# Performance work log

Measured on AMD Instinct MI355X. Metric: run time of the kernel, lower is better.

Reference implementation:

```python
import jax, jax.numpy as jnp
import numpy as np

NUM_NODES = 12288
NUM_GRAPHS = 1024
LEADS_PER_GRAPH = 12
SIG_LEN = 2048
NUM_EDGES = 196608


def _conv1d(x, w, b, stride, pad):
    # x: [N, C_in, L], w: [C_out, C_in, K]
    y = jax.lax.conv_general_dilated(
        x, w, window_strides=(stride,), padding=[(pad, pad)],
        dimension_numbers=("NCH", "OIH", "NCH"))
    return y + b[None, :, None]


def _gcn(x, src, dst, W, b, n_nodes):
    # PyG GCNConv: add self-loops, symmetric deg^-1/2 normalization.
    h = x @ W  # [N, out]
    loop = jnp.arange(n_nodes, dtype=src.dtype)
    s = jnp.concatenate([src, loop])
    d = jnp.concatenate([dst, loop])
    deg = jax.ops.segment_sum(jnp.ones(d.shape, h.dtype), d, num_segments=n_nodes)
    dis = jax.lax.rsqrt(deg)  # deg >= 1 due to self-loops
    norm = dis[s] * dis[d]  # [E+N]
    return jax.ops.segment_sum(h[s] * norm[:, None], d, num_segments=n_nodes) + b


def setup_inputs() -> dict:
    key = jax.random.key(0)
    ks = jax.random.split(key, 16)
    f = jnp.float32
    inp = {
        "x_raw": jax.random.normal(ks[0], (NUM_NODES, SIG_LEN), f),
        "conv1_w": jax.random.normal(ks[1], (16, 1, 7), f) * 0.2,
        "conv1_b": jax.random.normal(ks[2], (16,), f) * 0.05,
        "conv2_w": jax.random.normal(ks[3], (32, 16, 5), f) * 0.1,
        "conv2_b": jax.random.normal(ks[4], (32,), f) * 0.05,
        "lin_w": jax.random.normal(ks[5], (32, 64), f) * 0.15,
        "lin_b": jax.random.normal(ks[6], (64,), f) * 0.05,
        "gnn1_w": jax.random.normal(ks[7], (64, 128), f) * 0.1,
        "gnn1_b": jax.random.normal(ks[8], (128,), f) * 0.05,
        "gnn2_w": jax.random.normal(ks[9], (128, 128), f) * 0.08,
        "gnn2_b": jax.random.normal(ks[10], (128,), f) * 0.05,
        "fc_w": jax.random.normal(ks[11], (128, 5), f) * 0.08,
        "fc_b": jax.random.normal(ks[12], (5,), f) * 0.05,
        "edge_index": jax.random.randint(ks[13], (2, NUM_EDGES), 0, NUM_NODES, jnp.int32),
        "batch": (jnp.arange(NUM_NODES, dtype=jnp.int32) // LEADS_PER_GRAPH),
        "num_graphs": NUM_GRAPHS,
    }
    return inp


def reference(x_raw, conv1_w, conv1_b, conv2_w, conv2_b, lin_w, lin_b,
              gnn1_w, gnn1_b, gnn2_w, gnn2_b, fc_w, fc_b,
              edge_index, batch, num_graphs):
    n_nodes = x_raw.shape[0]
    # LeadCNN encoder
    h = x_raw[:, None, :]                              # [N,1,L]
    h = jax.nn.relu(_conv1d(h, conv1_w, conv1_b, 2, 3))  # [N,16,L/2]
    h = jax.nn.relu(_conv1d(h, conv2_w, conv2_b, 2, 2))  # [N,32,L/4]
    h = jnp.mean(h, axis=-1)                           # AdaptiveAvgPool1d(1)
    h = h @ lin_w + lin_b                              # [N,cnn_out]
    # Two GCN layers with ReLU
    src, dst = edge_index[0], edge_index[1]
    h = jax.nn.relu(_gcn(h, src, dst, gnn1_w, gnn1_b, n_nodes))
    h = jax.nn.relu(_gcn(h, src, dst, gnn2_w, gnn2_b, n_nodes))
    # global_mean_pool over batch
    sums = jax.ops.segment_sum(h, batch, num_segments=num_graphs)
    cnts = jax.ops.segment_sum(jnp.ones((n_nodes,), h.dtype), batch, num_segments=num_graphs)
    pooled = sums / jnp.maximum(cnts, 1.0)[:, None]
    return pooled @ fc_w + fc_b
```

## Files before the change

kernel.cpp:

```cpp
#include <hip/hip_runtime.h>
#include <cstddef>

#define N_NODES 12288
#define SIG     2048
#define C1N     16
#define L1N     1024
#define C2N     32
#define F0      64
#define F1      128
#define NEDGE   196608
#define NGRAPH  1024

#define NB_ENC   (N_NODES / 2)
#define CNT_BLKS (NEDGE / 256 + N_NODES / 256)

typedef float    f32x4 __attribute__((ext_vector_type(4)));
typedef _Float16 f16x8 __attribute__((ext_vector_type(8)));
typedef _Float16 f16x4 __attribute__((ext_vector_type(4)));
typedef __fp16   fp16x2_raw __attribute__((ext_vector_type(2)));

#if defined(__has_builtin)
#if __has_builtin(__builtin_amdgcn_mfma_f32_16x16x16f16)
#define HAVE_MFMA16 1
#endif
#endif

__device__ __forceinline__ unsigned pkrtz(float a, float b) {
    union { fp16x2_raw h; unsigned u; } c;
    c.h = __builtin_amdgcn_cvt_pkrtz(a, b);
    return c.u;
}

__global__ __launch_bounds__(256) void k_encoder(
    const float* __restrict__ x_raw,
    const float* __restrict__ conv1_w, const float* __restrict__ conv1_b,
    const float* __restrict__ conv2_w, const float* __restrict__ conv2_b,
    const float* __restrict__ lin_w,   const float* __restrict__ lin_b,
    float* __restrict__ h0,
    const int* __restrict__ dst, const int* __restrict__ batch,
    int* __restrict__ deg, float* __restrict__ cnt)
{
    __shared__ __align__(16) unsigned xw[2][1056];
    __shared__ __align__(16) unsigned c1t[4 * 800];
    __shared__ float wmsum[4][C2N];
    __shared__ float mean_s[2][C2N];

    const int tid = threadIdx.x;

    if (blockIdx.x >= NB_ENC) {
        const int b = blockIdx.x - NB_ENC;
        if (b < NEDGE / 256) {
            atomicAdd(&deg[dst[b * 256 + tid]], 1);
        } else {
            atomicAdd(&cnt[batch[(b - NEDGE / 256) * 256 + tid]], 1.f);
        }
        return;
    }

    const int lane = tid & 63;
    const int wq   = tid >> 6;
    const int colL = lane & 15;
    const int hi8  = lane >> 4;
    const int ndl  = wq >> 1;
    const int hf   = wq & 1;
    const int node = blockIdx.x * 2 + ndl;
    const float* xrow = x_raw + (size_t)node * SIG;
    unsigned* xn = &xw[ndl][0];

    const int nqu = hf ? 132 : 136;
    #pragma unroll
    for (int it = 0; it < 3; ++it) {
        int i = lane + 64 * it;
        if (i < nqu) {
            int xb = 1024 * hf + 8 * i - 8;
            float v[8];
            if (xb >= 0 && xb + 8 <= SIG) {
                float4 xa = *(const float4*)(xrow + xb);
                float4 xc = *(const float4*)(xrow + xb + 4);
                v[0] = xa.x; v[1] = xa.y; v[2] = xa.z; v[3] = xa.w;
                v[4] = xc.x; v[5] = xc.y; v[6] = xc.z; v[7] = xc.w;
            } else {
                #pragma unroll
                for (int t = 0; t < 8; ++t) {
                    int xi = xb + t;
                    v[t] = ((unsigned)xi < (unsigned)SIG) ? xrow[xi] : 0.f;
                }
            }
            uint4 w4;
            w4.x = pkrtz(v[0], v[1]); w4.y = pkrtz(v[2], v[3]);
            w4.z = pkrtz(v[4], v[5]); w4.w = pkrtz(v[6], v[7]);
            *(uint4*)&xn[512 * hf + 4 * i] = w4;
        }
    }
    if (hf == 1 && lane < 16) xn[1040 + lane] = 0u;

#if HAVE_MFMA16
    f16x4 w1A;
    #pragma unroll
    for (int j = 0; j < 4; ++j) w1A[j] = (_Float16)0.f;
    if (hi8 == 0) {
        #pragma unroll
        for (int j = 1; j < 4; ++j) w1A[j] = (_Float16)conv1_w[colL * 7 + (j - 1)];
    } else if (hi8 == 1) {
        #pragma unroll
        for (int j = 0; j < 4; ++j) w1A[j] = (_Float16)conv1_w[colL * 7 + 3 + j];
    }
#else
    f16x8 w1A;
    #pragma unroll
    for (int j = 0; j < 8; ++j) w1A[j] = (_Float16)0.f;
    if (hi8 == 0) {
        #pragma unroll
        for (int j = 1; j < 8; ++j) w1A[j] = (_Float16)conv1_w[colL * 7 + (j - 1)];
    }
#endif
    float bias1[4];
    #pragma unroll
    for (int r = 0; r < 4; ++r) bias1[r] = conv1_b[hi8 * 4 + r];

    f16x8 wA[2][3];
    #pragma unroll
    for (int mt = 0; mt < 2; ++mt) {
        const int oc = mt * 16 + colL;
        #pragma unroll
        for (int kt = 0; kt < 3; ++kt) {
            #pragma unroll
            for (int j = 0; j < 8; ++j) {
                const int ic  = 4 * hi8 + (j & 3);
                const int tap = 2 * kt + (j >> 2);
                wA[mt][kt][j] = (_Float16)((tap < 5) ? conv2_w[oc * 80 + ic * 5 + tap] : 0.f);
            }
        }
    }
    float bias2[2][4];
    #pragma unroll
    for (int mt = 0; mt < 2; ++mt)
        #pragma unroll
        for (int r = 0; r < 4; ++r)
            bias2[mt][r] = conv2_b[mt * 16 + hi8 * 4 + r];

    float msumr[2][4];
    #pragma unroll
    for (int mt = 0; mt < 2; ++mt)
        #pragma unroll
        for (int r = 0; r < 4; ++r) msumr[mt][r] = 0.f;

    unsigned* cw = &c1t[wq * 800];
    const int rb = 20 * colL + 4 * hi8;

    #pragma unroll 1
    for (int sp = 0; sp < 8; ++sp) {
        const int xwb = 512 * hf + 64 * sp;

        #pragma unroll
        for (int T = 0; T < 5; ++T) {
            f32x4 a;
            a[0] = bias1[0]; a[1] = bias1[1]; a[2] = bias1[2]; a[3] = bias1[3];
#if HAVE_MFMA16
            const int wbase = xwb + 16 * T + colL + 2 * hi8;
            union { unsigned u[2]; f16x4 v; } Bx;
            Bx.u[0] = xn[wbase];
            Bx.u[1] = xn[wbase + 1];
            a = __builtin_amdgcn_mfma_f32_16x16x16f16(w1A, Bx.v, a, 0, 0, 0);
#else
            const int wbase = xwb + 16 * T + colL + 4 * hi8;
            union { unsigned u[4]; f16x8 v; } Bx;
            #pragma unroll
            for (int u = 0; u < 4; ++u) Bx.u[u] = xn[wbase + u];
            a = __builtin_amdgcn_mfma_f32_16x16x32_f16(w1A, Bx.v, a, 0, 0, 0);
#endif
            uint2 wr;
            wr.x = pkrtz(fmaxf(a[0], 0.f), fmaxf(a[1], 0.f));
            wr.y = pkrtz(fmaxf(a[2], 0.f), fmaxf(a[3], 0.f));
            const int slot = 16 * T + colL;
            *(uint2*)&cw[(slot >> 1) * 20 + 4 * hi8 + (slot & 1) * 2] = wr;
        }
        if (hf == 0 && sp == 0) {
            if (lane < 16) cw[lane] = 0u;
        }
        if (hf == 1 && sp == 7) {
            for (int k2 = lane; k2 < 140; k2 += 64) cw[660 + k2] = 0u;
        }

        #pragma unroll
        for (int nt = 0; nt < 2; ++nt) {
            f32x4 acc[2];
            #pragma unroll
            for (int mt = 0; mt < 2; ++mt) {
                acc[mt][0] = bias2[mt][0]; acc[mt][1] = bias2[mt][1];
                acc[mt][2] = bias2[mt][2]; acc[mt][3] = bias2[mt][3];
            }
            #pragma unroll
            for (int kt = 0; kt < 3; ++kt) {
                union { uint4 u4; f16x8 v; } B;
                B.u4 = *(const uint4*)&cw[rb + 320 * nt + 20 * kt];
                #pragma unroll
                for (int mt = 0; mt < 2; ++mt)
                    acc[mt] = __builtin_amdgcn_mfma_f32_16x16x32_f16(wA[mt][kt], B.v, acc[mt], 0, 0, 0);
            }
            #pragma unroll
            for (int mt = 0; mt < 2; ++mt)
                #pragma unroll
                for (int r = 0; r < 4; ++r)
                    msumr[mt][r] += fmaxf(acc[mt][r], 0.f);
        }
    }

    #pragma unroll
    for (int mt = 0; mt < 2; ++mt)
        #pragma unroll
        for (int r = 0; r < 4; ++r) {
            float s = msumr[mt][r];
            s += __shfl_xor(s, 1);
            s += __shfl_xor(s, 2);
            s += __shfl_xor(s, 4);
            s += __shfl_xor(s, 8);
            msumr[mt][r] = s;
        }
    if (colL == 0) {
        #pragma unroll
        for (int mt = 0; mt < 2; ++mt)
            #pragma unroll
            for (int r = 0; r < 4; ++r)
                wmsum[wq][mt * 16 + hi8 * 4 + r] = msumr[mt][r];
    }
    __syncthreads();

    if (tid < 64) {
        const int nd2 = tid >> 5, oc = tid & 31;
        mean_s[nd2][oc] = (wmsum[2 * nd2][oc] + wmsum[2 * nd2 + 1][oc]) * (1.f / 512.f);
    }
    __syncthreads();

    if (tid < 128) {
        const int nd2 = tid >> 6, o = tid & 63;
        const int nodew = blockIdx.x * 2 + nd2;
        float a = lin_b[o];
        #pragma unroll
        for (int ic = 0; ic < C2N; ++ic)
            a = fmaf(mean_s[nd2][ic], lin_w[ic * F0 + o], a);
        h0[(size_t)nodew * F0 + o] = a;
    }
}

__global__ __launch_bounds__(1024) void k_scan(const int* __restrict__ deg,
                                               int* __restrict__ rowptr,
                                               int* __restrict__ cursor,
                                               float* __restrict__ dis,
                                               float* __restrict__ invd)
{
    __shared__ int wtot[16];
    const int t = threadIdx.x;
    const int lane = t & 63, wvid = t >> 6;
    int d[12]; int s = 0;
    #pragma unroll
    for (int m = 0; m < 12; ++m) { d[m] = deg[12 * t + m]; s += d[m]; }
    const int mysum = s;
    #pragma unroll
    for (int off = 1; off < 64; off <<= 1) {
        int u = __shfl_up(s, off);
        if (lane >= off) s += u;
    }
    if (lane == 63) wtot[wvid] = s;
    __syncthreads();
    if (t < 16) {
        int v = wtot[t];
        #pragma unroll
        for (int off = 1; off < 16; off <<= 1) {
            int u = __shfl_up(v, off);
            if (t >= off) v += u;
        }
        wtot[t] = v;
    }
    __syncthreads();
    int run = (wvid ? wtot[wvid - 1] : 0) + (s - mysum);
    if (t == 0) rowptr[0] = 0;
    #pragma unroll
    for (int m = 0; m < 12; ++m) {
        const int i = 12 * t + m;
        cursor[i] = run;
        run += d[m];
        rowptr[i + 1] = run;
        float df = (float)(d[m] + 1);
        dis[i]  = rsqrtf(df);
        invd[i] = 1.f / df;
    }
}

__global__ __launch_bounds__(256) void k_scatter(const int* __restrict__ src,
                                                 const int* __restrict__ dst,
                                                 int* __restrict__ cursor,
                                                 int* __restrict__ csr)
{
    int e = blockIdx.x * 256 + threadIdx.x;
    if (e < NEDGE) {
        int d = dst[e];
        int idx = atomicAdd(&cursor[d], 1);
        csr[idx] = src[e];
    }
}

template <int K, int POOL>
__global__ __launch_bounds__(256) void k_gcn(
    const float* __restrict__ h, const int* __restrict__ rowptr,
    const int* __restrict__ csr, const float* __restrict__ dis,
    const float* __restrict__ invd, const float* __restrict__ W,
    const float* __restrict__ bvec, float* __restrict__ out,
    const int* __restrict__ batch, float* __restrict__ pooled)
{
    __shared__ float hs[8][K];
    const int tid = threadIdx.x;
    const int n0  = blockIdx.x * 8;

    const int npb = 256 / K;
    const int f   = tid & (K - 1);
    const int sub = tid / K;
    #pragma unroll
    for (int it = 0; it < 8 / npb; ++it) {
        const int nl = it * npb + sub;
        const int n  = n0 + nl;
        const float dn = dis[n];
        float a0 = h[(size_t)n * K + f] * invd[n];
        float a1 = 0.f, a2 = 0.f, a3 = 0.f;
        int e = rowptr[n];
        const int e1 = rowptr[n + 1];
        for (; e + 3 < e1; e += 4) {
            int s0 = csr[e], s1 = csr[e + 1], s2 = csr[e + 2], s3 = csr[e + 3];
            a0 = fmaf(h[(size_t)s0 * K + f], dis[s0] * dn, a0);
            a1 = fmaf(h[(size_t)s1 * K + f], dis[s1] * dn, a1);
            a2 = fmaf(h[(size_t)s2 * K + f], dis[s2] * dn, a2);
            a3 = fmaf(h[(size_t)s3 * K + f], dis[s3] * dn, a3);
        }
        for (; e < e1; ++e) {
            int s0 = csr[e];
            a0 = fmaf(h[(size_t)s0 * K + f], dis[s0] * dn, a0);
        }
        hs[nl][f] = (a0 + a1) + (a2 + a3);
    }
    __syncthreads();

    const int j    = tid & 127;
    const int half = tid >> 7;
    float a[4];
    #pragma unroll
    for (int c = 0; c < 4; ++c) a[c] = bvec[j];

    for (int k4 = 0; k4 < K; k4 += 4) {
        float w0 = W[(k4 + 0) * F1 + j];
        float w1 = W[(k4 + 1) * F1 + j];
        float w2 = W[(k4 + 2) * F1 + j];
        float w3 = W[(k4 + 3) * F1 + j];
        #pragma unroll
        for (int c = 0; c < 4; ++c) {
            float4 hv = *(const float4*)&hs[half * 4 + c][k4];
            a[c] = fmaf(hv.x, w0, a[c]);
            a[c] = fmaf(hv.y, w1, a[c]);
            a[c] = fmaf(hv.z, w2, a[c]);
            a[c] = fmaf(hv.w, w3, a[c]);
        }
    }
    #pragma unroll
    for (int c = 0; c < 4; ++c) {
        float r = fmaxf(a[c], 0.f);
        int n = n0 + half * 4 + c;
        if (POOL) atomicAdd(&pooled[(size_t)batch[n] * F1 + j], r);
        else      out[(size_t)n * F1 + j] = r;
    }
}

__global__ __launch_bounds__(128) void k_final(const float* __restrict__ pooled,
                                               const float* __restrict__ cnt,
                                               const float* __restrict__ fc_w,
                                               const float* __restrict__ fc_b,
                                               float* __restrict__ out)
{
    __shared__ float ps[F1];
    const int g = blockIdx.x, tid = threadIdx.x;
    float inv = 1.f / fmaxf(cnt[g], 1.f);
    ps[tid] = pooled[g * F1 + tid] * inv;
    __syncthreads();
    if (tid < 5) {
        float a = fc_b[tid];
        for (int f = 0; f < F1; ++f) a = fmaf(ps[f], fc_w[f * 5 + tid], a);
        out[g * 5 + tid] = a;
    }
}

extern "C" void kernel_launch(void* const* d_in, const int* in_sizes, int n_in,
                              void* d_out, int out_size, void* d_ws, size_t ws_size,
                              hipStream_t stream)
{
    const float* x_raw = (const float*)d_in[0];
    const float* c1w   = (const float*)d_in[1];
    const float* c1b   = (const float*)d_in[2];
    const float* c2w   = (const float*)d_in[3];
    const float* c2b   = (const float*)d_in[4];
    const float* lw    = (const float*)d_in[5];
    const float* lb    = (const float*)d_in[6];
    const float* g1w   = (const float*)d_in[7];
    const float* g1b   = (const float*)d_in[8];
    const float* g2w   = (const float*)d_in[9];
    const float* g2b   = (const float*)d_in[10];
    const float* fcw   = (const float*)d_in[11];
    const float* fcb   = (const float*)d_in[12];
    const int*   ei    = (const int*)d_in[13];
    const int*   batch = (const int*)d_in[14];
    const int* src = ei;
    const int* dst = ei + NEDGE;

    float* ws = (float*)d_ws;
    float* h0     = ws + 0;
    float* h1     = ws + 786432;
    float* dis    = ws + 2359296;
    float* invd   = ws + 2371584;
    float* pooled = ws + 2383872;
    float* cnt    = ws + 2514944;
    int*   deg    = (int*)(ws + 2515968);
    int*   rowptr = (int*)(ws + 2528256);
    int*   cursor = (int*)(ws + 2540548);
    int*   csr    = (int*)(ws + 2552836);

    float* out = (float*)d_out;

    hipMemsetAsync(deg, 0, N_NODES * sizeof(int), stream);
    hipMemsetAsync(pooled, 0, (size_t)(NGRAPH * F1 + NGRAPH) * sizeof(float), stream);

    k_encoder<<<NB_ENC + CNT_BLKS, 256, 0, stream>>>(
        x_raw, c1w, c1b, c2w, c2b, lw, lb, h0, dst, batch, deg, cnt);
    k_scan<<<1, 1024, 0, stream>>>(deg, rowptr, cursor, dis, invd);
    k_scatter<<<NEDGE / 256, 256, 0, stream>>>(src, dst, cursor, csr);

    k_gcn<F0, 0><<<N_NODES / 8, 256, 0, stream>>>(h0, rowptr, csr, dis, invd, g1w, g1b, h1, batch, pooled);
    k_gcn<F1, 1><<<N_NODES / 8, 256, 0, stream>>>(h1, rowptr, csr, dis, invd, g2w, g2b, nullptr, batch, pooled);

    k_final<<<NGRAPH, 128, 0, stream>>>(pooled, cnt, fcw, fcb, out);
}
```

Before: 154.9 us.

## Store GCN layer-1 output as fp16 and shrink encoder LDS footprint

Layer-1 GCN output is now packed to fp16 pairs, which halves the bytes gathered per edge in the layer-2 aggregation; layer 2 unpacks the pairs and accumulates in fp32. The encoder's conv1 tile buffer shrinks from 800 to 680 words per wave, with the reduction scratch aliased into it behind an added barrier, to cut LDS use and possibly raise occupancy. ReLU after conv1 is applied with a packed fp16 max, and the unused tail tile writes are skipped. The fp16 intermediate adds rounding error to the layer-2 inputs.

Measured after the change: 177.8 us. +14.8%, slower.

```diff
diff --git a/kernel.cpp b/kernel.cpp
--- a/kernel.cpp
+++ b/kernel.cpp
@@ -13,6 +13,7 @@
 
 #define NB_ENC   (N_NODES / 2)
 #define CNT_BLKS (NEDGE / 256 + N_NODES / 256)
+#define C1TW     680
 
 typedef float    f32x4 __attribute__((ext_vector_type(4)));
 typedef _Float16 f16x8 __attribute__((ext_vector_type(8)));
@@ -29,6 +30,18 @@
     union { fp16x2_raw h; unsigned u; } c;
     c.h = __builtin_amdgcn_cvt_pkrtz(a, b);
     return c.u;
+}
+__device__ __forceinline__ unsigned pkmax0(unsigned x) {
+    unsigned r;
+    asm("v_pk_max_f16 %0, %1, 0" : "=v"(r) : "v"(x));
+    return r;
+}
+__device__ __forceinline__ unsigned short f16_bits(float f) {
+    union { _Float16 h; unsigned short u; } c; c.h = (_Float16)f; return c.u;
+}
+__device__ __forceinline__ float2 unpk16(unsigned u) {
+    union { unsigned v; _Float16 h[2]; } c; c.v = u;
+    return make_float2((float)c.h[0], (float)c.h[1]);
 }
 
 __global__ __launch_bounds__(256) void k_encoder(
@@ -41,9 +54,9 @@
     int* __restrict__ deg, float* __restrict__ cnt)
 {
     __shared__ __align__(16) unsigned xw[2][1056];
-    __shared__ __align__(16) unsigned c1t[4 * 800];
-    __shared__ float wmsum[4][C2N];
-    __shared__ float mean_s[2][C2N];
+    __shared__ __align__(16) unsigned c1t[4 * C1TW];
+    float* wmsum  = (float*)&c1t[0];
+    float* mean_s = (float*)&c1t[128];
 
     const int tid = threadIdx.x;
 
@@ -145,7 +158,7 @@
         #pragma unroll
         for (int r = 0; r < 4; ++r) msumr[mt][r] = 0.f;
 
-    unsigned* cw = &c1t[wq * 800];
+    unsigned* cw = &c1t[wq * C1TW];
     const int rb = 20 * colL + 4 * hi8;
 
     #pragma unroll 1
@@ -170,16 +183,17 @@
             a = __builtin_amdgcn_mfma_f32_16x16x32_f16(w1A, Bx.v, a, 0, 0, 0);
 #endif
             uint2 wr;
-            wr.x = pkrtz(fmaxf(a[0], 0.f), fmaxf(a[1], 0.f));
-            wr.y = pkrtz(fmaxf(a[2], 0.f), fmaxf(a[3], 0.f));
+            wr.x = pkmax0(pkrtz(a[0], a[1]));
+            wr.y = pkmax0(pkrtz(a[2], a[3]));
             const int slot = 16 * T + colL;
-            *(uint2*)&cw[(slot >> 1) * 20 + 4 * hi8 + (slot & 1) * 2] = wr;
+            if (T < 4 || colL < 4)
+                *(uint2*)&cw[(slot >> 1) * 20 + 4 * hi8 + (slot & 1) * 2] = wr;
         }
         if (hf == 0 && sp == 0) {
             if (lane < 16) cw[lane] = 0u;
         }
         if (hf == 1 && sp == 7) {
-            for (int k2 = lane; k2 < 140; k2 += 64) cw[660 + k2] = 0u;
+            if (lane < 20) cw[660 + lane] = 0u;
         }
 
         #pragma unroll
@@ -217,18 +231,20 @@
             s += __shfl_xor(s, 8);
             msumr[mt][r] = s;
         }
+    __syncthreads();
     if (colL == 0) {
         #pragma unroll
         for (int mt = 0; mt < 2; ++mt)
             #pragma unroll
             for (int r = 0; r < 4; ++r)
-                wmsum[wq][mt * 16 + hi8 * 4 + r] = msumr[mt][r];
+                wmsum[wq * 32 + mt * 16 + hi8 * 4 + r] = msumr[mt][r];
     }
     __syncthreads();
 
     if (tid < 64) {
         const int nd2 = tid >> 5, oc = tid & 31;
-        mean_s[nd2][oc] = (wmsum[2 * nd2][oc] + wmsum[2 * nd2 + 1][oc]) * (1.f / 512.f);
+        mean_s[nd2 * 32 + oc] =
+            (wmsum[(2 * nd2) * 32 + oc] + wmsum[(2 * nd2 + 1) * 32 + oc]) * (1.f / 512.f);
     }
     __syncthreads();
 
@@ -238,7 +254,7 @@
         float a = lin_b[o];
         #pragma unroll
         for (int ic = 0; ic < C2N; ++ic)
-            a = fmaf(mean_s[nd2][ic], lin_w[ic * F0 + o], a);
+            a = fmaf(mean_s[nd2 * 32 + ic], lin_w[ic * F0 + o], a);
         h0[(size_t)nodew * F0 + o] = a;
     }
 }
@@ -300,40 +316,37 @@
     }
 }
 
-template <int K, int POOL>
-__global__ __launch_bounds__(256) void k_gcn(
+__global__ __launch_bounds__(256) void k_gcn1(
     const float* __restrict__ h, const int* __restrict__ rowptr,
     const int* __restrict__ csr, const float* __restrict__ dis,
     const float* __restrict__ invd, const float* __restrict__ W,
-    const float* __restrict__ bvec, float* __restrict__ out,
-    const int* __restrict__ batch, float* __restrict__ pooled)
-{
-    __shared__ float hs[8][K];
+    const float* __restrict__ bvec, unsigned* __restrict__ h1h)
+{
+    __shared__ float hs[8][F0];
     const int tid = threadIdx.x;
     const int n0  = blockIdx.x * 8;
 
-    const int npb = 256 / K;
-    const int f   = tid & (K - 1);
-    const int sub = tid / K;
-    #pragma unroll
-    for (int it = 0; it < 8 / npb; ++it) {
-        const int nl = it * npb + sub;
+    const int f   = tid & 63;
+    const int sub = tid >> 6;
+    #pragma unroll
+    for (int it = 0; it < 2; ++it) {
+        const int nl = it * 4 + sub;
         const int n  = n0 + nl;
         const float dn = dis[n];
-        float a0 = h[(size_t)n * K + f] * invd[n];
+        float a0 = h[(size_t)n * F0 + f] * invd[n];
         float a1 = 0.f, a2 = 0.f, a3 = 0.f;
         int e = rowptr[n];
         const int e1 = rowptr[n + 1];
         for (; e + 3 < e1; e += 4) {
             int s0 = csr[e], s1 = csr[e + 1], s2 = csr[e + 2], s3 = csr[e + 3];
-            a0 = fmaf(h[(size_t)s0 * K + f], dis[s0] * dn, a0);
-            a1 = fmaf(h[(size_t)s1 * K + f], dis[s1] * dn, a1);
-            a2 = fmaf(h[(size_t)s2 * K + f], dis[s2] * dn, a2);
-            a3 = fmaf(h[(size_t)s3 * K + f], dis[s3] * dn, a3);
+            a0 = fmaf(h[(size_t)s0 * F0 + f], dis[s0] * dn, a0);
+            a1 = fmaf(h[(size_t)s1 * F0 + f], dis[s1] * dn, a1);
+            a2 = fmaf(h[(size_t)s2 * F0 + f], dis[s2] * dn, a2);
+            a3 = fmaf(h[(size_t)s3 * F0 + f], dis[s3] * dn, a3);
         }
         for (; e < e1; ++e) {
             int s0 = csr[e];
-            a0 = fmaf(h[(size_t)s0 * K + f], dis[s0] * dn, a0);
+            a0 = fmaf(h[(size_t)s0 * F0 + f], dis[s0] * dn, a0);
         }
         hs[nl][f] = (a0 + a1) + (a2 + a3);
     }
@@ -345,7 +358,7 @@
     #pragma unroll
     for (int c = 0; c < 4; ++c) a[c] = bvec[j];
 
-    for (int k4 = 0; k4 < K; k4 += 4) {
+    for (int k4 = 0; k4 < F0; k4 += 4) {
         float w0 = W[(k4 + 0) * F1 + j];
         float w1 = W[(k4 + 1) * F1 + j];
         float w2 = W[(k4 + 2) * F1 + j];
@@ -361,10 +374,88 @@
     }
     #pragma unroll
     for (int c = 0; c < 4; ++c) {
+        float r  = fmaxf(a[c], 0.f);
+        float rn = __shfl_down(r, 1);
+        if ((j & 1) == 0) {
+            int n = n0 + half * 4 + c;
+            h1h[(size_t)n * 64 + (j >> 1)] =
+                (unsigned)f16_bits(r) | ((unsigned)f16_bits(rn) << 16);
+        }
+    }
+}
+
+__global__ __launch_bounds__(256) void k_gcn2(
+    const unsigned* __restrict__ h1h, const int* __restrict__ rowptr,
+    const int* __restrict__ csr, const float* __restrict__ dis,
+    const float* __restrict__ invd, const float* __restrict__ W,
+    const float* __restrict__ bvec, const int* __restrict__ batch,
+    float* __restrict__ pooled)
+{
+    __shared__ float hs[8][F1];
+    const int tid = threadIdx.x;
+    const int n0  = blockIdx.x * 8;
+
+    const int f2  = tid & 63;
+    const int sub = tid >> 6;
+    #pragma unroll
+    for (int it = 0; it < 2; ++it) {
+        const int nl = it * 4 + sub;
+        const int n  = n0 + nl;
+        const float dn = dis[n];
+        float2 sf = unpk16(h1h[(size_t)n * 64 + f2]);
+        float a0 = sf.x * invd[n], b0 = sf.y * invd[n];
+        float a1 = 0.f, b1 = 0.f, a2 = 0.f, b2 = 0.f, a3 = 0.f, b3 = 0.f;
+        int e = rowptr[n];
+        const int e1 = rowptr[n + 1];
+        for (; e + 3 < e1; e += 4) {
+            int s0 = csr[e], s1 = csr[e + 1], s2 = csr[e + 2], s3 = csr[e + 3];
+            float w0 = dis[s0] * dn, w1 = dis[s1] * dn;
+            float w2 = dis[s2] * dn, w3 = dis[s3] * dn;
+            float2 v0 = unpk16(h1h[(size_t)s0 * 64 + f2]);
+            float2 v1 = unpk16(h1h[(size_t)s1 * 64 + f2]);
+            float2 v2 = unpk16(h1h[(size_t)s2 * 64 + f2]);
+            float2 v3 = unpk16(h1h[(size_t)s3 * 64 + f2]);
+            a0 = fmaf(v0.x, w0, a0); b0 = fmaf(v0.y, w0, b0);
+            a1 = fmaf(v1.x, w1, a1); b1 = fmaf(v1.y, w1, b1);
+            a2 = fmaf(v2.x, w2, a2); b2 = fmaf(v2.y, w2, b2);
+            a3 = fmaf(v3.x, w3, a3); b3 = fmaf(v3.y, w3, b3);
+        }
+        for (; e < e1; ++e) {
+            int s0 = csr[e];
+            float w0 = dis[s0] * dn;
+            float2 v0 = unpk16(h1h[(size_t)s0 * 64 + f2]);
+            a0 = fmaf(v0.x, w0, a0); b0 = fmaf(v0.y, w0, b0);
+        }
+        *(float2*)&hs[nl][2 * f2] =
+            make_float2((a0 + a1) + (a2 + a3), (b0 + b1) + (b2 + b3));
+    }
+    __syncthreads();
+
+    const int j    = tid & 127;
+    const int half = tid >> 7;
+    float a[4];
+    #pragma unroll
+    for (int c = 0; c < 4; ++c) a[c] = bvec[j];
+
+    for (int k4 = 0; k4 < F1; k4 += 4) {
+        float w0 = W[(k4 + 0) * F1 + j];
+        float w1 = W[(k4 + 1) * F1 + j];
+        float w2 = W[(k4 + 2) * F1 + j];
+        float w3 = W[(k4 + 3) * F1 + j];
+        #pragma unroll
+        for (int c = 0; c < 4; ++c) {
+            float4 hv = *(const float4*)&hs[half * 4 + c][k4];
+            a[c] = fmaf(hv.x, w0, a[c]);
+            a[c] = fmaf(hv.y, w1, a[c]);
+            a[c] = fmaf(hv.z, w2, a[c]);
+            a[c] = fmaf(hv.w, w3, a[c]);
+        }
+    }
+    #pragma unroll
+    for (int c = 0; c < 4; ++c) {
         float r = fmaxf(a[c], 0.f);
         int n = n0 + half * 4 + c;
-        if (POOL) atomicAdd(&pooled[(size_t)batch[n] * F1 + j], r);
-        else      out[(size_t)n * F1 + j] = r;
+        atomicAdd(&pooled[(size_t)batch[n] * F1 + j], r);
     }
 }
 
@@ -409,16 +500,16 @@
     const int* dst = ei + NEDGE;
 
     float* ws = (float*)d_ws;
-    float* h0     = ws + 0;
-    float* h1     = ws + 786432;
-    float* dis    = ws + 2359296;
-    float* invd   = ws + 2371584;
-    float* pooled = ws + 2383872;
-    float* cnt    = ws + 2514944;
-    int*   deg    = (int*)(ws + 2515968);
-    int*   rowptr = (int*)(ws + 2528256);
-    int*   cursor = (int*)(ws + 2540548);
-    int*   csr    = (int*)(ws + 2552836);
+    float*    h0     = ws + 0;
+    unsigned* h1h    = (unsigned*)(ws + 786432);
+    float*    dis    = ws + 1572864;
+    float*    invd   = ws + 1585152;
+    float*    pooled = ws + 1597440;
+    float*    cnt    = ws + 1728512;
+    int*      deg    = (int*)(ws + 1729536);
+    int*      rowptr = (int*)(ws + 1741824);
+    int*      cursor = (int*)(ws + 1754116);
+    int*      csr    = (int*)(ws + 1766404);
 
     float* out = (float*)d_out;
 
@@ -430,8 +521,8 @@
     k_scan<<<1, 1024, 0, stream>>>(deg, rowptr, cursor, dis, invd);
     k_scatter<<<NEDGE / 256, 256, 0, stream>>>(src, dst, cursor, csr);
 
-    k_gcn<F0, 0><<<N_NODES / 8, 256, 0, stream>>>(h0, rowptr, csr, dis, invd, g1w, g1b, h1, batch, pooled);
-    k_gcn<F1, 1><<<N_NODES / 8, 256, 0, stream>>>(h1, rowptr, csr, dis, invd, g2w, g2b, nullptr, batch, pooled);
+    k_gcn1<<<N_NODES / 8, 256, 0, stream>>>(h0, rowptr, csr, dis, invd, g1w, g1b, h1h);
+    k_gcn2<<<N_NODES / 8, 256, 0, stream>>>(h1h, rowptr, csr, dis, invd, g2w, g2b, batch, pooled);
 
     k_final<<<NGRAPH, 128, 0, stream>>>(pooled, cnt, fcw, fcb, out);
 }
```
